# Performance work log

Measured on AMD Instinct MI355X. Metric: run time of the kernel, lower is better.

## Reference

```python
import jax, jax.numpy as jnp
import numpy as np

N_HEAD = 16
N_KV_HEADS = 4
N_REP = 4
HEAD_DIM = 128
N_EMBD = 2048
EPS = 1e-5
ROPE_BASE = 10000.0


def setup_inputs() -> dict:
    key = jax.random.key(0)
    ks = jax.random.split(key, 5)
    B, T, C = 2, 2048, N_EMBD
    s = 0.02
    return {
        "x": jax.random.normal(ks[0], (B, T, C), dtype=jnp.float32),
        "wq": jax.random.normal(ks[1], (C, N_HEAD * HEAD_DIM), dtype=jnp.float32) * s,
        "wk": jax.random.normal(ks[2], (C, N_KV_HEADS * HEAD_DIM), dtype=jnp.float32) * s,
        "wv": jax.random.normal(ks[3], (C, N_KV_HEADS * HEAD_DIM), dtype=jnp.float32) * s,
        "wc": jax.random.normal(ks[4], (C, C), dtype=jnp.float32) * s,
        "q_norm_w": jnp.ones((HEAD_DIM,), dtype=jnp.float32),
        "k_norm_w": jnp.ones((HEAD_DIM,), dtype=jnp.float32),
    }


def _rmsnorm(x, w):
    # norm in fp32, scale by weight (matches RMSNorm.forward)
    xf = x.astype(jnp.float32)
    rms = jax.lax.rsqrt(jnp.mean(xf * xf, axis=-1, keepdims=True) + EPS)
    return (xf * rms).astype(x.dtype) * w


def _rope(x, cos, sin):
    # x: [B,T,H,D]; cos/sin: [T, D//2]; interleaved even/odd rotation
    xf = x.astype(jnp.float32)
    xe = xf[..., 0::2]
    xo = xf[..., 1::2]
    c = cos[None, :, None, :]
    s = sin[None, :, None, :]
    ye = xe * c - xo * s
    yo = xe * s + xo * c
    y = jnp.stack((ye, yo), axis=-1).reshape(x.shape)
    return y.astype(x.dtype)


def reference(x, wq, wk, wv, wc, q_norm_w, k_norm_w):
    B, T, C = x.shape
    q = (x @ wq).reshape(B, T, N_HEAD, HEAD_DIM)
    k = (x @ wk).reshape(B, T, N_KV_HEADS, HEAD_DIM)
    v = (x @ wv).reshape(B, T, N_KV_HEADS, HEAD_DIM)

    q = _rmsnorm(q, q_norm_w)
    k = _rmsnorm(k, k_norm_w)

    inv_freq = 1.0 / (ROPE_BASE ** (jnp.arange(0, HEAD_DIM, 2, dtype=jnp.float32) / HEAD_DIM))
    theta = jnp.arange(T, dtype=jnp.float32)[:, None] * inv_freq[None, :]  # [T, D//2]
    cos, sin = jnp.cos(theta), jnp.sin(theta)
    q = _rope(q, cos, sin)
    k = _rope(k, cos, sin)

    # GQA: repeat kv heads (repeat_kv with n_rep)
    k = jnp.repeat(k, N_REP, axis=2)  # [B,T,H,D]
    v = jnp.repeat(v, N_REP, axis=2)

    scale = 1.0 / jnp.sqrt(jnp.float32(HEAD_DIM))
    scores = jnp.einsum("bthd,bshd->bhts", q, k) * scale  # [B,H,T,S]
    causal = jnp.tril(jnp.ones((T, T), dtype=bool))
    scores = jnp.where(causal[None, None], scores, jnp.finfo(scores.dtype).min)
    attn = jax.nn.softmax(scores, axis=-1)
    y = jnp.einsum("bhts,bshd->bthd", attn, v).reshape(B, T, C)
    return y @ wc
```

## Files before the change

kernel.cpp:

```cpp
#include <hip/hip_runtime.h>
#include <hip/hip_bf16.h>
#include <cstdint>
#include <cstddef>

using bf16 = __hip_bfloat16;
typedef __attribute__((ext_vector_type(8))) short short8;
typedef __attribute__((ext_vector_type(4))) float f32x4;
typedef __attribute__((ext_vector_type(16))) float f32x16;

#define T_SEQ 2048
#define NHEAD 16
#define NKV 4
#define HD 128
#define CE 2048

__device__ __forceinline__ void gl_lds16(const void* g, void* l) {
  __builtin_amdgcn_global_load_lds(
      (const __attribute__((address_space(1))) unsigned int*)g,
      (__attribute__((address_space(3))) unsigned int*)l, 16, 0, 0);
}

__device__ __forceinline__ unsigned int cvtpk_bf16(float lo, float hi) {
  unsigned int r;
  asm("v_cvt_pk_bf16_f32 %0, %1, %2" : "=v"(r) : "v"(lo), "v"(hi));
  return r;
}

__device__ __forceinline__ void plswap(unsigned int& x, unsigned int& y, int hi) {
#if __has_builtin(__builtin_amdgcn_permlane32_swap)
  auto r = __builtin_amdgcn_permlane32_swap(x, y, false, false);
  x = r[0];
  y = r[1];
#else
  unsigned int xp = (unsigned int)__shfl_xor((int)x, 32);
  unsigned int yp = (unsigned int)__shfl_xor((int)y, 32);
  unsigned int nx = hi ? yp : x;
  unsigned int ny = hi ? y : xp;
  x = nx;
  y = ny;
#endif
}

__global__ void __launch_bounds__(256) cvt_bf16(const float* __restrict__ in,
                                                bf16* __restrict__ out, int n4) {
  const int i = blockIdx.x * blockDim.x + threadIdx.x;
  if (i >= n4) return;
  const float4 v = ((const float4*)in)[i];
  bf16 b0 = __float2bfloat16(v.x), b1 = __float2bfloat16(v.y),
       b2 = __float2bfloat16(v.z), b3 = __float2bfloat16(v.w);
  ushort4 u;
  u.x = *(const unsigned short*)&b0; u.y = *(const unsigned short*)&b1;
  u.z = *(const unsigned short*)&b2; u.w = *(const unsigned short*)&b3;
  ((ushort4*)out)[i] = u;
}

__global__ void __launch_bounds__(256) transpose_cvt(const float* __restrict__ W,
                                                     bf16* __restrict__ Wt, int N) {
  __shared__ float tile[32][33];
  const int tx = threadIdx.x & 31, ty = threadIdx.x >> 5;
  const int bx = blockIdx.x, by = blockIdx.y;
#pragma unroll
  for (int i = 0; i < 4; i++) {
    const int r = by * 32 + ty + i * 8;
    tile[ty + i * 8][tx] = W[(size_t)r * N + bx * 32 + tx];
  }
  __syncthreads();
#pragma unroll
  for (int i = 0; i < 4; i++) {
    const int n = bx * 32 + ty + i * 8;
    Wt[(size_t)n * 2048 + by * 32 + tx] = __float2bfloat16(tile[tx][ty + i * 8]);
  }
}

#define LOADA(mh)                                                              \
  _Pragma("unroll") for (int i = 0; i < MF / 2; i++) {                         \
    const int lrow = wr * (BM / WM) + ((mh) * (MF / 2) + i) * 16 + l15;        \
    _Pragma("unroll") for (int kk = 0; kk < 2; kk++) {                         \
      areg[i][kk] = *(const short8*)(sA + lrow * 64 +                          \
                    ((((kk << 2) | l4) ^ (lrow & 7)) << 3));                   \
    }                                                                          \
  }

#define LOADB(nh)                                                              \
  _Pragma("unroll") for (int j = 0; j < NF / 2; j++) {                         \
    const int lrow = wc * (BN / WN) + ((nh) * (NF / 2) + j) * 16 + l15;        \
    _Pragma("unroll") for (int kk = 0; kk < 2; kk++) {                         \
      breg[j][kk] = *(const short8*)(sB + lrow * 64 +                          \
                    ((((kk << 2) | l4) ^ (lrow & 7)) << 3));                   \
    }                                                                          \
  }

#define MFMAQ(mh, nh)                                                          \
  __builtin_amdgcn_s_setprio(1);                                               \
  _Pragma("unroll") for (int i = 0; i < MF / 2; i++)                           \
  _Pragma("unroll") for (int j = 0; j < NF / 2; j++)                           \
  _Pragma("unroll") for (int kk = 0; kk < 2; kk++)                             \
    acc[(mh) * (MF / 2) + i][(nh) * (NF / 2) + j] =                            \
        __builtin_amdgcn_mfma_f32_16x16x32_bf16(                               \
            areg[i][kk], breg[j][kk],                                          \
            acc[(mh) * (MF / 2) + i][(nh) * (NF / 2) + j], 0, 0, 0);           \
  __builtin_amdgcn_s_setprio(0);

template <int BM, int BN, int WM, int WN>
__global__ void __launch_bounds__(512, 2)
gemm8p(const bf16* __restrict__ A, const bf16* __restrict__ Bt,
       float* __restrict__ C, int M, int N, int K) {
  constexpr int MF = BM / WM / 16;
  constexpr int NF = BN / WN / 16;
  constexpr int AL = BM / 64;
  constexpr int BL = BN / 64;
  __shared__ bf16 smA[2][BM * 64];
  __shared__ bf16 smB[2][BN * 64];

  const int tid = threadIdx.x, lane = tid & 63, wid = tid >> 6;
  const int l15 = lane & 15, l4 = lane >> 4;
  const int wr = wid / WN, wc = wid % WN;

  const int nwg = gridDim.x;
  const int q = nwg >> 3, r = nwg & 7;
  const int xcd = blockIdx.x & 7, lin = blockIdx.x >> 3;
  const int wg = (xcd < r ? xcd * (q + 1) : r * (q + 1) + (xcd - r) * q) + lin;
  const int gw = N / BN;
  const int by = wg / gw, bx = wg % gw;
  const int row0 = by * BM, col0 = bx * BN;
  const int NT = K >> 6;

  const bf16* Ag = A + (size_t)row0 * K;
  const bf16* Bg = Bt + (size_t)col0 * K;

  auto stageA = [&](int t, int pbuf) {
    const int k0 = t << 6;
#pragma unroll
    for (int j = 0; j < AL; j++) {
      const int c = j * 512 + tid;
      const int rowi = c >> 3;
      gl_lds16(Ag + (size_t)rowi * K + k0 + (((c & 7) ^ (rowi & 7)) << 3),
               (void*)(&smA[pbuf][c << 3]));
    }
  };
  auto stageB = [&](int t, int pbuf) {
    const int k0 = t << 6;
#pragma unroll
    for (int j = 0; j < BL; j++) {
      const int c = j * 512 + tid;
      const int rowi = c >> 3;
      gl_lds16(Bg + (size_t)rowi * K + k0 + (((c & 7) ^ (rowi & 7)) << 3),
               (void*)(&smB[pbuf][c << 3]));
    }
  };

  f32x4 acc[MF][NF];
#pragma unroll
  for (int i = 0; i < MF; i++)
#pragma unroll
    for (int j = 0; j < NF; j++) acc[i][j] = (f32x4){0.f, 0.f, 0.f, 0.f};
  short8 areg[MF / 2][2], breg[NF / 2][2];

  stageA(0, 0);
  stageB(0, 0);
  stageA(1, 1);
  asm volatile("s_waitcnt vmcnt(%0)" ::"i"(AL) : "memory");
  __builtin_amdgcn_s_barrier();

  for (int t = 0; t < NT; ++t) {
    const int buf = t & 1;
    const bf16* sA = smA[buf];
    const bf16* sB = smB[buf];
    const int tB = (t + 1 < NT) ? t + 1 : NT - 1;
    const int tA = (t + 2 < NT) ? t + 2 : NT - 1;

    stageB(tB, buf ^ 1);
    LOADA(0)
    LOADB(0)
    __builtin_amdgcn_s_barrier();
    MFMAQ(0, 0)
    __builtin_amdgcn_s_barrier();
    LOADB(1)
    __builtin_amdgcn_s_barrier();
    MFMAQ(0, 1)
    __builtin_amdgcn_s_barrier();
    LOADA(1)
    __builtin_amdgcn_s_barrier();
    MFMAQ(1, 1)
    __builtin_amdgcn_s_barrier();
    stageA(tA, buf);
    LOADB(0)
    asm volatile("s_waitcnt vmcnt(%0)" ::"i"(AL) : "memory");
    __builtin_amdgcn_s_barrier();
    MFMAQ(1, 0)
    __builtin_amdgcn_s_barrier();
  }

#pragma unroll
  for (int i = 0; i < MF; i++)
#pragma unroll
    for (int j = 0; j < NF; j++)
#pragma unroll
      for (int rr = 0; rr < 4; rr++)
        C[(size_t)(row0 + wr * (BM / WM) + i * 16 + l4 * 4 + rr) * N +
          (col0 + wc * (BN / WN) + j * 16 + l15)] = acc[i][j][rr];
}

__global__ void __launch_bounds__(256) qkv_post(const float* __restrict__ QKV,
                                                const float* __restrict__ qw,
                                                const float* __restrict__ kw,
                                                bf16* __restrict__ Qo,
                                                bf16* __restrict__ Ko,
                                                bf16* __restrict__ Vto) {
  const int g = blockIdx.x * 4 + (threadIdx.x >> 6);
  const int lane = threadIdx.x & 63;
  const int hh = g % 24;
  const int bt = g / 24;
  const int b = bt >> 11, t = bt & (T_SEQ - 1);
  int off;
  if (hh < 16) off = hh * 128;
  else if (hh < 20) off = 2048 + (hh - 16) * 128;
  else off = 2560 + (hh - 20) * 128;
  const float2 x = *(const float2*)(QKV + (size_t)bt * 3072 + off + lane * 2);
  if (hh < 20) {
    float ss = x.x * x.x + x.y * x.y;
    ss += __shfl_xor(ss, 1);  ss += __shfl_xor(ss, 2);  ss += __shfl_xor(ss, 4);
    ss += __shfl_xor(ss, 8);  ss += __shfl_xor(ss, 16); ss += __shfl_xor(ss, 32);
    const float rms = rsqrtf(ss * (1.0f / 128.0f) + 1e-5f);
    const float* w = (hh < 16) ? qw : kw;
    const float x0 = x.x * rms * w[lane * 2];
    const float x1 = x.y * rms * w[lane * 2 + 1];
    const float inv = exp2f((float)lane * (-13.287712379549449f / 64.0f));
    const float th = (float)t * inv;
    const float sn = sinf(th), cs = cosf(th);
    const float y0 = x0 * cs - x1 * sn;
    const float y1 = x0 * sn + x1 * cs;
    const bf16 o0 = __float2bfloat16(y0), o1 = __float2bfloat16(y1);
    if (hh < 16) {
      bf16* d = Qo + ((size_t)(b * NHEAD + hh) * T_SEQ + t) * HD + lane * 2;
      d[0] = o0; d[1] = o1;
    } else {
      bf16* d = Ko + ((size_t)(b * NKV + (hh - 16)) * T_SEQ + t) * HD + lane * 2;
      d[0] = o0; d[1] = o1;
    }
  } else {
    bf16* d = Vto + ((size_t)(b * NKV + (hh - 20)) * HD + lane * 2) * T_SEQ + t;
    d[0] = __float2bfloat16(x.x);
    d[T_SEQ] = __float2bfloat16(x.y);
  }
}

__global__ void __launch_bounds__(256, 2) attn_fwd(const bf16* __restrict__ Q,
                                                   const bf16* __restrict__ K,
                                                   const bf16* __restrict__ Vt,
                                                   bf16* __restrict__ Y) {
  __shared__ bf16 smK[128 * 128];
  __shared__ bf16 smV[128 * 128];

  const int bid = blockIdx.x;
  const int p = bid & 255, sdx = bid >> 8;
  const int bh = p & 31;
  const int jh = p >> 5;
  const int jq = sdx ? (15 - jh) : jh;
  const int h = bh & (NHEAD - 1), b = bh >> 4;
  const int bkv = b * NKV + (h >> 2);

  const int tid = threadIdx.x, wid = tid >> 6, lane = tid & 63;
  const int l31 = lane & 31, hi = lane >> 5;
  const int q0w = jq * 128 + wid * 32;

  const bf16* Kb = K + (size_t)bkv * T_SEQ * HD;
  const bf16* Vb = Vt + (size_t)bkv * HD * T_SEQ;

  const bf16* Qrow = Q + ((size_t)bh * T_SEQ + q0w + l31) * HD + hi * 8;
  short8 qf[8];
#pragma unroll
  for (int ds = 0; ds < 8; ds++) qf[ds] = *(const short8*)(Qrow + ds * 16);

  f32x16 o[4];
#pragma unroll
  for (int d = 0; d < 4; d++) o[d] = (f32x16)(0.f);
  float mrun = -INFINITY, lrun = 0.f;

  constexpr float CL = 0.08838834764831845f * 1.44269504088896340736f;
  const int trow = tid >> 4, tslot = tid & 15;

  for (int t = 0; t <= jq; t++) {
    const int k0 = t * 128;
    __syncthreads();
#pragma unroll
    for (int i = 0; i < 8; i++) {
      const int row = i * 16 + trow;
      const int ss = (tslot ^ (row & 15)) * 8;
      gl_lds16(Kb + (size_t)(k0 + row) * HD + ss, (void*)((char*)smK + i * 4096 + wid * 1024));
      gl_lds16(Vb + (size_t)row * T_SEQ + k0 + ss, (void*)((char*)smV + i * 4096 + wid * 1024));
    }
    __syncthreads();

    const bool lastt = (t == jq);
    const int glim = lastt ? wid : 3;

    f32x16 sg[4];
#pragma unroll
    for (int g = 0; g < 4; g++) {
      if (g > glim) continue;
      f32x16 acc = (f32x16)(0.f);
#pragma unroll
      for (int ds = 0; ds < 8; ds++) {
        const int row = g * 32 + l31;
        const short8 kf = *(const short8*)(smK + (size_t)row * 128 +
                                           (((ds << 1) | hi) ^ (row & 15)) * 8);
        acc = __builtin_amdgcn_mfma_f32_32x32x16_bf16(kf, qf[ds], acc, 0, 0, 0);
      }
      sg[g] = acc;
    }
    float tmax = -INFINITY;
#pragma unroll
    for (int g = 0; g < 4; g++) {
      if (g > glim) continue;
      if (lastt && g == wid) {
#pragma unroll
        for (int r = 0; r < 16; r++) {
          const int kr = (r & 3) + 8 * (r >> 2) + (hi << 2);
          if (kr > l31) sg[g][r] = -INFINITY;
        }
      }
#pragma unroll
      for (int r = 0; r < 16; r++) tmax = fmaxf(tmax, sg[g][r]);
    }
    tmax = fmaxf(tmax, __shfl_xor(tmax, 32));
    const float mnew = fmaxf(mrun, tmax);
    const float f = exp2f((mrun - mnew) * CL);
    mrun = mnew;
    lrun *= f;
#pragma unroll
    for (int d = 0; d < 4; d++)
#pragma unroll
      for (int r = 0; r < 16; r++) o[d][r] *= f;

    float lsum = 0.f;
#pragma unroll
    for (int g = 0; g < 4; g++) {
      if (g > glim) continue;
      float pp[16];
      float s0 = 0.f, s1 = 0.f;
#pragma unroll
      for (int r = 0; r < 16; r++) pp[r] = exp2f((sg[g][r] - mnew) * CL);
#pragma unroll
      for (int r = 0; r < 8; r++) { s0 += pp[2 * r]; s1 += pp[2 * r + 1]; }
      lsum += s0 + s1;

      unsigned int w0 = cvtpk_bf16(pp[0], pp[1]),  w2 = cvtpk_bf16(pp[4], pp[5]);
      unsigned int w1 = cvtpk_bf16(pp[2], pp[3]),  w3 = cvtpk_bf16(pp[6], pp[7]);
      unsigned int w4 = cvtpk_bf16(pp[8], pp[9]),  w6 = cvtpk_bf16(pp[12], pp[13]);
      unsigned int w5 = cvtpk_bf16(pp[10], pp[11]), w7 = cvtpk_bf16(pp[14], pp[15]);
      plswap(w0, w2, hi); plswap(w1, w3, hi);
      plswap(w4, w6, hi); plswap(w5, w7, hi);
      union { unsigned int u[4]; short8 s8; } pa0, pa1;
      pa0.u[0] = w0; pa0.u[1] = w1; pa0.u[2] = w2; pa0.u[3] = w3;
      pa1.u[0] = w4; pa1.u[1] = w5; pa1.u[2] = w6; pa1.u[3] = w7;

#pragma unroll
      for (int d = 0; d < 4; d++) {
        const int row = d * 32 + l31;
        const int ks0 = g * 2, ks1 = g * 2 + 1;
        const short8 vf0 = *(const short8*)(smV + (size_t)row * 128 +
                                            (((ks0 << 1) | hi) ^ (row & 15)) * 8);
        const short8 vf1 = *(const short8*)(smV + (size_t)row * 128 +
                                            (((ks1 << 1) | hi) ^ (row & 15)) * 8);
        o[d] = __builtin_amdgcn_mfma_f32_32x32x16_bf16(vf0, pa0.s8, o[d], 0, 0, 0);
        o[d] = __builtin_amdgcn_mfma_f32_32x32x16_bf16(vf1, pa1.s8, o[d], 0, 0, 0);
      }
    }
    lrun += lsum + __shfl_xor(lsum, 32);
  }

  const float inv = 1.0f / lrun;
  bf16* yrow = Y + ((size_t)(b * T_SEQ + q0w + l31)) * CE + h * HD;
#pragma unroll
  for (int d = 0; d < 4; d++) {
#pragma unroll
    for (int rg = 0; rg < 4; rg++) {
      ushort4 u;
      bf16 e0 = __float2bfloat16(o[d][rg * 4 + 0] * inv);
      bf16 e1 = __float2bfloat16(o[d][rg * 4 + 1] * inv);
      bf16 e2 = __float2bfloat16(o[d][rg * 4 + 2] * inv);
      bf16 e3 = __float2bfloat16(o[d][rg * 4 + 3] * inv);
      u.x = *(const unsigned short*)&e0; u.y = *(const unsigned short*)&e1;
      u.z = *(const unsigned short*)&e2; u.w = *(const unsigned short*)&e3;
      *(ushort4*)(yrow + d * 32 + rg * 8 + (hi << 2)) = u;
    }
  }
}

extern "C" void kernel_launch(void* const* d_in, const int* in_sizes, int n_in,
                              void* d_out, int out_size, void* d_ws, size_t ws_size,
                              hipStream_t stream) {
  const float* x   = (const float*)d_in[0];
  const float* wq  = (const float*)d_in[1];
  const float* wk  = (const float*)d_in[2];
  const float* wv  = (const float*)d_in[3];
  const float* wc  = (const float*)d_in[4];
  const float* qnw = (const float*)d_in[5];
  const float* knw = (const float*)d_in[6];
  float* out = (float*)d_out;

  char* ws = (char*)d_ws;
  bf16*  xb    = (bf16*)(ws);
  bf16*  wqkvt = (bf16*)(ws + 16777216);
  bf16*  wct   = (bf16*)(ws + 29360128);
  float* qkv   = (float*)(ws + 37748736);
  bf16*  Qb    = (bf16*)(ws + 88080384);
  bf16*  Kb    = (bf16*)(ws + 104857600);
  bf16*  Vtb   = (bf16*)(ws + 109051904);
  bf16*  yb    = (bf16*)(ws + 113246208);

  cvt_bf16<<<8192, 256, 0, stream>>>(x, xb, 2097152);
  transpose_cvt<<<dim3(64, 64), 256, 0, stream>>>(wq, wqkvt, 2048);
  transpose_cvt<<<dim3(16, 64), 256, 0, stream>>>(wk, wqkvt + (size_t)2048 * 2048, 512);
  transpose_cvt<<<dim3(16, 64), 256, 0, stream>>>(wv, wqkvt + (size_t)2560 * 2048, 512);
  transpose_cvt<<<dim3(64, 64), 256, 0, stream>>>(wc, wct, 2048);
  gemm8p<256, 256, 2, 4><<<192, 512, 0, stream>>>(xb, wqkvt, qkv, 4096, 3072, 2048);
  qkv_post<<<24576, 256, 0, stream>>>(qkv, qnw, knw, Qb, Kb, Vtb);
  attn_fwd<<<512, 256, 0, stream>>>(Qb, Kb, Vtb, yb);
  gemm8p<256, 128, 4, 2><<<256, 512, 0, stream>>>(yb, wct, out, 4096, 2048, 2048);
}
```

Before: 240.6 us.

## Replace 8-phase GEMM schedule with 2-barrier schedule and smaller M tiles

The GEMM main loop drops the eight barrier-separated load/MFMA phases. It now loads all B fragments and half of A up front, runs the MFMA quadrants with only two barriers per k-step, and overlaps the A staging with the last quadrant. Both GEMMs switch to 128x256 tiles with 2x4 warps, which raises the QKV grid to 384 blocks and changes the output projection tiling. Fewer barriers should cut synchronisation stalls, but holding all B fragments in registers raises register pressure, and smaller M tiles reduce data reuse per block.

```diff
diff --git a/kernel.cpp b/kernel.cpp
--- a/kernel.cpp
+++ b/kernel.cpp
@@ -72,41 +72,13 @@
   }
 }
 
-#define LOADA(mh)                                                              \
-  _Pragma("unroll") for (int i = 0; i < MF / 2; i++) {                         \
-    const int lrow = wr * (BM / WM) + ((mh) * (MF / 2) + i) * 16 + l15;        \
-    _Pragma("unroll") for (int kk = 0; kk < 2; kk++) {                         \
-      areg[i][kk] = *(const short8*)(sA + lrow * 64 +                          \
-                    ((((kk << 2) | l4) ^ (lrow & 7)) << 3));                   \
-    }                                                                          \
-  }
-
-#define LOADB(nh)                                                              \
-  _Pragma("unroll") for (int j = 0; j < NF / 2; j++) {                         \
-    const int lrow = wc * (BN / WN) + ((nh) * (NF / 2) + j) * 16 + l15;        \
-    _Pragma("unroll") for (int kk = 0; kk < 2; kk++) {                         \
-      breg[j][kk] = *(const short8*)(sB + lrow * 64 +                          \
-                    ((((kk << 2) | l4) ^ (lrow & 7)) << 3));                   \
-    }                                                                          \
-  }
-
-#define MFMAQ(mh, nh)                                                          \
-  __builtin_amdgcn_s_setprio(1);                                               \
-  _Pragma("unroll") for (int i = 0; i < MF / 2; i++)                           \
-  _Pragma("unroll") for (int j = 0; j < NF / 2; j++)                           \
-  _Pragma("unroll") for (int kk = 0; kk < 2; kk++)                             \
-    acc[(mh) * (MF / 2) + i][(nh) * (NF / 2) + j] =                            \
-        __builtin_amdgcn_mfma_f32_16x16x32_bf16(                               \
-            areg[i][kk], breg[j][kk],                                          \
-            acc[(mh) * (MF / 2) + i][(nh) * (NF / 2) + j], 0, 0, 0);           \
-  __builtin_amdgcn_s_setprio(0);
-
 template <int BM, int BN, int WM, int WN>
 __global__ void __launch_bounds__(512, 2)
-gemm8p(const bf16* __restrict__ A, const bf16* __restrict__ Bt,
+gemm2p(const bf16* __restrict__ A, const bf16* __restrict__ Bt,
        float* __restrict__ C, int M, int N, int K) {
   constexpr int MF = BM / WM / 16;
   constexpr int NF = BN / WN / 16;
+  constexpr int MH = MF / 2, NH = NF / 2;
   constexpr int AL = BM / 64;
   constexpr int BL = BN / 64;
   __shared__ bf16 smA[2][BM * 64];
@@ -154,7 +126,8 @@
   for (int i = 0; i < MF; i++)
 #pragma unroll
     for (int j = 0; j < NF; j++) acc[i][j] = (f32x4){0.f, 0.f, 0.f, 0.f};
-  short8 areg[MF / 2][2], breg[NF / 2][2];
+
+  short8 a0[MH][2], a1[MH][2], bR[NF][2];
 
   stageA(0, 0);
   stageB(0, 0);
@@ -170,24 +143,78 @@
     const int tA = (t + 2 < NT) ? t + 2 : NT - 1;
 
     stageB(tB, buf ^ 1);
-    LOADA(0)
-    LOADB(0)
-    __builtin_amdgcn_s_barrier();
-    MFMAQ(0, 0)
-    __builtin_amdgcn_s_barrier();
-    LOADB(1)
-    __builtin_amdgcn_s_barrier();
-    MFMAQ(0, 1)
-    __builtin_amdgcn_s_barrier();
-    LOADA(1)
-    __builtin_amdgcn_s_barrier();
-    MFMAQ(1, 1)
+
+#pragma unroll
+    for (int i = 0; i < MH; i++)
+#pragma unroll
+      for (int kk = 0; kk < 2; kk++) {
+        const int lrow = wr * (BM / WM) + i * 16 + l15;
+        a0[i][kk] = *(const short8*)(sA + lrow * 64 +
+                                     ((((kk << 2) | l4) ^ (lrow & 7)) << 3));
+      }
+#pragma unroll
+    for (int j = 0; j < NF; j++)
+#pragma unroll
+      for (int kk = 0; kk < 2; kk++) {
+        const int lrow = wc * (BN / WN) + j * 16 + l15;
+        bR[j][kk] = *(const short8*)(sB + lrow * 64 +
+                                     ((((kk << 2) | l4) ^ (lrow & 7)) << 3));
+      }
+
+    __builtin_amdgcn_s_setprio(1);
+#pragma unroll
+    for (int i = 0; i < MH; i++)
+#pragma unroll
+      for (int j = 0; j < NH; j++)
+#pragma unroll
+        for (int kk = 0; kk < 2; kk++)
+          acc[i][j] = __builtin_amdgcn_mfma_f32_16x16x32_bf16(
+              a0[i][kk], bR[j][kk], acc[i][j], 0, 0, 0);
+    __builtin_amdgcn_s_setprio(0);
+
+#pragma unroll
+    for (int i = 0; i < MH; i++)
+#pragma unroll
+      for (int kk = 0; kk < 2; kk++) {
+        const int lrow = wr * (BM / WM) + (MH + i) * 16 + l15;
+        a1[i][kk] = *(const short8*)(sA + lrow * 64 +
+                                     ((((kk << 2) | l4) ^ (lrow & 7)) << 3));
+      }
+
+    __builtin_amdgcn_s_setprio(1);
+#pragma unroll
+    for (int i = 0; i < MH; i++)
+#pragma unroll
+      for (int j = 0; j < NH; j++)
+#pragma unroll
+        for (int kk = 0; kk < 2; kk++)
+          acc[i][NH + j] = __builtin_amdgcn_mfma_f32_16x16x32_bf16(
+              a0[i][kk], bR[NH + j][kk], acc[i][NH + j], 0, 0, 0);
+#pragma unroll
+    for (int i = 0; i < MH; i++)
+#pragma unroll
+      for (int j = 0; j < NH; j++)
+#pragma unroll
+        for (int kk = 0; kk < 2; kk++)
+          acc[MH + i][NH + j] = __builtin_amdgcn_mfma_f32_16x16x32_bf16(
+              a1[i][kk], bR[NH + j][kk], acc[MH + i][NH + j], 0, 0, 0);
+    __builtin_amdgcn_s_setprio(0);
+
     __builtin_amdgcn_s_barrier();
     stageA(tA, buf);
-    LOADB(0)
+
+    __builtin_amdgcn_s_setprio(1);
+#pragma unroll
+    for (int i = 0; i < MH; i++)
+#pragma unroll
+      for (int j = 0; j < NH; j++)
+#pragma unroll
+        for (int kk = 0; kk < 2; kk++)
+          acc[MH + i][j] = __builtin_amdgcn_mfma_f32_16x16x32_bf16(
+              a1[i][kk], bR[j][kk], acc[MH + i][j], 0, 0, 0);
+    __builtin_amdgcn_s_setprio(0);
+
     asm volatile("s_waitcnt vmcnt(%0)" ::"i"(AL) : "memory");
-    __builtin_amdgcn_s_barrier();
-    MFMAQ(1, 0)
     __builtin_amdgcn_s_barrier();
   }
 
@@ -199,6 +226,8 @@
       for (int rr = 0; rr < 4; rr++)
         C[(size_t)(row0 + wr * (BM / WM) + i * 16 + l4 * 4 + rr) * N +
           (col0 + wc * (BN / WN) + j * 16 + l15)] = acc[i][j][rr];
+
+  asm volatile("s_waitcnt vmcnt(0)" ::: "memory");
 }
 
 __global__ void __launch_bounds__(256) qkv_post(const float* __restrict__ QKV,
@@ -415,8 +444,8 @@
   transpose_cvt<<<dim3(16, 64), 256, 0, stream>>>(wk, wqkvt + (size_t)2048 * 2048, 512);
   transpose_cvt<<<dim3(16, 64), 256, 0, stream>>>(wv, wqkvt + (size_t)2560 * 2048, 512);
   transpose_cvt<<<dim3(64, 64), 256, 0, stream>>>(wc, wct, 2048);
-  gemm8p<256, 256, 2, 4><<<192, 512, 0, stream>>>(xb, wqkvt, qkv, 4096, 3072, 2048);
+  gemm2p<128, 256, 2, 4><<<384, 512, 0, stream>>>(xb, wqkvt, qkv, 4096, 3072, 2048);
   qkv_post<<<24576, 256, 0, stream>>>(qkv, qnw, knw, Qb, Kb, Vtb);
   attn_fwd<<<512, 256, 0, stream>>>(Qb, Kb, Vtb, yb);
-  gemm8p<256, 128, 4, 2><<<256, 512, 0, stream>>>(yb, wct, out, 4096, 2048, 2048);
-}
+  gemm2p<128, 256, 2, 4><<<256, 512, 0, stream>>>(yb, wct, out, 4096, 2048, 2048);
+}
```

New measurement: 250.4 us. +4.1%, slower.
